# Performance work log

Hardware: AMD Instinct MI355X
Metric: run time of the kernel (lower is better)

Reference implementation:

```python
import jax, jax.numpy as jnp
import numpy as np

B, N, F, K = 4, 512, 128, 32
GAMMA = 10.0          # RBF width parameter
CUTOFF = 5.0          # RBF center range [0, CUTOFF]
LOG2 = 0.6931471805599453
EPS = 1e-12           # keeps sqrt grad finite on the (masked-out) diagonal


def ssp(x):
    # shifted softplus: ln(0.5*e^x + 0.5) = softplus(x) - ln 2
    return jax.nn.softplus(x) - LOG2


def setup_inputs() -> dict:
    key = jax.random.key(0)
    ks = jax.random.split(key, 8)
    coordinates = jax.random.normal(ks[0], (B, N, 3), dtype=jnp.float32) * 3.0
    atom_emb = jax.random.normal(ks[1], (B, N, F), dtype=jnp.float32)
    rbf_centers = jnp.linspace(0.0, CUTOFF, K, dtype=jnp.float32)
    # cfconv filter-generator dense layers
    w1 = jax.random.normal(ks[2], (K, F), dtype=jnp.float32) / np.float32(np.sqrt(K))
    b1 = jnp.zeros((F,), dtype=jnp.float32)
    w2 = jax.random.normal(ks[3], (F, F), dtype=jnp.float32) / np.float32(np.sqrt(F))
    b2 = jnp.zeros((F,), dtype=jnp.float32)
    # self.W linear (nn.Linear stores weight as [out, in])
    Ww = jax.random.normal(ks[4], (F, F), dtype=jnp.float32) / np.float32(np.sqrt(F))
    Wb = jnp.zeros((F,), dtype=jnp.float32)
    return {"coordinates": coordinates, "atom_emb": atom_emb,
            "rbf_centers": rbf_centers, "w1": w1, "b1": b1,
            "w2": w2, "b2": b2, "Ww": Ww, "Wb": Wb}


def reference(coordinates, atom_emb, rbf_centers, w1, b1, w2, b2, Ww, Wb):
    n = coordinates.shape[-2]
    # pairwise distances [B, N, N]
    diff = coordinates[:, :, None, :] - coordinates[:, None, :, :]
    d = jnp.sqrt(jnp.sum(diff * diff, axis=-1) + EPS)
    # Gaussian RBF expansion [B, N, N, K]
    rbf = jnp.exp(-GAMMA * (d[..., None] - rbf_centers) ** 2)
    # filter generator: Dense -> SSP -> Dense -> SSP  => W [B, N, N, F]
    Wf = ssp(jnp.einsum('bnmk,kf->bnmf', rbf, w1) + b1)
    Wf = ssp(jnp.einsum('bnmf,fg->bnmg', Wf, w2) + b2)
    # zero the diagonal (no self-interaction)
    mask = (1.0 - jnp.eye(n, dtype=Wf.dtype))[None, :, :, None]
    Wf = Wf * mask
    # x = self.W(atom_emb)
    x = atom_emb @ Ww.T + Wb
    # per-channel weighted neighbor aggregation
    x = jnp.einsum('bnmf,bmf->bnf', Wf, x)
    return atom_emb + x
```

## Files before the change

### kernel.cpp

```cpp
#include <hip/hip_runtime.h>
#include <hip/hip_bf16.h>

#define B_ 4
#define N_ 512
#define F_ 128
#define K_ 32
#define TD 2048
#define DMAX 6.5f
#define XWB (B_ * N_ / 2)
#define TKEEPI 1890

typedef __attribute__((ext_vector_type(4))) float f32x4;

__device__ __forceinline__ unsigned cvt_pk_bf16(float a, float b) {
  unsigned r;
  asm("v_cvt_pk_bf16_f32 %0, %1, %2" : "=v"(r) : "v"(a), "v"(b));
  return r;
}
__device__ __forceinline__ unsigned short f2bf1(float a) {
  return (unsigned short)cvt_pk_bf16(a, a);
}
__device__ __forceinline__ float exp2_hw(float x) {
  float r; asm("v_exp_f32 %0, %1" : "=v"(r) : "v"(x)); return r;
}
__device__ __forceinline__ float log2_hw(float x) {
  float r; asm("v_log_f32 %0, %1" : "=v"(r) : "v"(x)); return r;
}
__device__ __forceinline__ float lo16f(unsigned w) {
  return __builtin_bit_cast(float, w << 16);
}
__device__ __forceinline__ float hi16f(unsigned w) {
  return __builtin_bit_cast(float, w & 0xffff0000u);
}

__device__ __forceinline__ float sspb(float u) {
  float e = exp2_hw(__builtin_fabsf(u) * -1.4426950408889634f);
  float l = log2_hw(fmaf(e, 0.5f, 0.5f));
  return fmaf(l, 0.6931471805599453f, fmaxf(u, 0.f));
}

__launch_bounds__(256)
__global__ void prep_kernel(const float* __restrict__ emb, const float* __restrict__ Ww,
                            const float* __restrict__ Wb,
                            const float* __restrict__ w1, const float* __restrict__ b1,
                            const float* __restrict__ w2, const float* __restrict__ b2,
                            unsigned short* __restrict__ xbf,
                            unsigned short* __restrict__ tabn) {
  __shared__ float erow[2][F_];
  __shared__ float rbf_s[2][K_];
  __shared__ float h1s[2][F_];

  if (blockIdx.x < XWB) {
    const int r0 = blockIdx.x * 2;
    const int half = threadIdx.x >> 7, f = threadIdx.x & 127;
    erow[half][f] = emb[(r0 + half) * F_ + f];
    __syncthreads();
    const float4* w4 = (const float4*)(Ww + f * F_);
    const float* er = erow[half];
    float acc = 0.f;
#pragma unroll 8
    for (int g4 = 0; g4 < F_ / 4; ++g4) {
      float4 wv = w4[g4];
      acc = fmaf(er[g4 * 4 + 0], wv.x, acc);
      acc = fmaf(er[g4 * 4 + 1], wv.y, acc);
      acc = fmaf(er[g4 * 4 + 2], wv.z, acc);
      acc = fmaf(er[g4 * 4 + 3], wv.w, acc);
    }
    xbf[(r0 + half) * F_ + f] = f2bf1(acc + Wb[f]);
  } else {
    const int j = blockIdx.x - XWB;
    const int sl = threadIdx.x >> 7, f = threadIdx.x & 127;
    const int i = 2 * j + sl;
    const float d = (float)i * (DMAX / (float)(TD - 1));
    if (f < K_) {
      float t = d - (float)f * (5.0f / 31.0f);
      rbf_s[sl][f] = exp2_hw(t * t * -14.426950408889634f);
    }
    __syncthreads();
    float a1 = b1[f];
#pragma unroll 8
    for (int k = 0; k < K_; ++k) a1 = fmaf(rbf_s[sl][k], w1[k * F_ + f], a1);
    h1s[sl][f] = sspb(a1);
    __syncthreads();
    float a2 = b2[f];
#pragma unroll 8
    for (int g = 0; g < F_; ++g) a2 = fmaf(h1s[sl][g], w2[g * F_ + f], a2);
    tabn[i * F_ + f] = f2bf1(sspb(a2));
  }
}

__launch_bounds__(256, 5)
__global__ void agg_kernel(const float* __restrict__ coords, const float* __restrict__ emb,
                           const unsigned short* __restrict__ xbf,
                           const unsigned short* __restrict__ tabn,
                           float* __restrict__ out) {
  __shared__ unsigned cidx[N_ + 96];
  __shared__ unsigned wcnt[4];
  __shared__ float part[16][F_ + 4];

  const int blk = blockIdx.x;
  const int b = blk >> 9, n = blk & 511;
  const int tid = threadIdx.x;
  const int lane = tid & 63, wq = tid >> 6;

  const float cx = coords[(b * N_ + n) * 3 + 0];
  const float cy = coords[(b * N_ + n) * 3 + 1];
  const float cz = coords[(b * N_ + n) * 3 + 2];

  const float SC = (float)(TD - 1) / DMAX;
  const int mA = wq * 128 + lane;
  const int mB = mA + 64;
  unsigned vA, vB;
  bool keepA, keepB;
  {
    const float* cm = coords + (b * N_ + mA) * 3;
    float dx = cm[0] - cx, dy = cm[1] - cy, dz = cm[2] - cz;
    float d = sqrtf(fmaf(dx, dx, fmaf(dy, dy, fmaf(dz, dz, 1e-12f))));
    int ti = (int)fminf(fmaf(d, SC, 0.5f), (float)(TD - 1));
    vA = ((unsigned)ti << 16) | (unsigned)mA;
    keepA = (ti < TKEEPI) && (mA != n);
  }
  {
    const float* cm = coords + (b * N_ + mB) * 3;
    float dx = cm[0] - cx, dy = cm[1] - cy, dz = cm[2] - cz;
    float d = sqrtf(fmaf(dx, dx, fmaf(dy, dy, fmaf(dz, dz, 1e-12f))));
    int ti = (int)fminf(fmaf(d, SC, 0.5f), (float)(TD - 1));
    vB = ((unsigned)ti << 16) | (unsigned)mB;
    keepB = (ti < TKEEPI) && (mB != n);
  }
  unsigned long long bA = __ballot(keepA);
  unsigned long long bB = __ballot(keepB);
  if (lane == 0) wcnt[wq] = (unsigned)(__popcll(bA) + __popcll(bB));
  __syncthreads();
  const unsigned c0 = wcnt[0], c1 = wcnt[1], c2 = wcnt[2], c3 = wcnt[3];
  const int cnt = (int)(c0 + c1 + c2 + c3);
  {
    unsigned pre = (wq > 0 ? c0 : 0u) + (wq > 1 ? c1 : 0u) + (wq > 2 ? c2 : 0u);
    unsigned long long below = (1ull << lane) - 1ull;
    unsigned posA = pre + (unsigned)__popcll(bA & below);
    unsigned posB = pre + (unsigned)__popcll(bA) + (unsigned)__popcll(bB & below);
    if (keepA) cidx[posA] = vA;
    if (keepB) cidx[posB] = vB;
    if (tid < 96) cidx[cnt + tid] = ((unsigned)(TD - 1)) << 16;
  }
  __syncthreads();

  const int mg = tid >> 4;
  const int f0 = (tid & 15) * 8;
  const unsigned short* xp = xbf + b * N_ * F_ + f0;
  const unsigned short* tp = tabn + f0;

  f32x4 acc0 = {0.f, 0.f, 0.f, 0.f};
  f32x4 acc1 = {0.f, 0.f, 0.f, 0.f};

#define LOADP(V, T, X)                                                       \
  {                                                                          \
    unsigned v_ = (V);                                                       \
    T = *(const uint4*)(tp + (v_ >> 16) * F_);                               \
    X = *(const uint4*)(xp + (v_ & 0xffffu) * F_);                           \
  }
#define MAC8(T, X)                                                           \
  {                                                                          \
    acc0[0] = fmaf(lo16f(T.x), lo16f(X.x), acc0[0]);                         \
    acc0[1] = fmaf(hi16f(T.x), hi16f(X.x), acc0[1]);                         \
    acc0[2] = fmaf(lo16f(T.y), lo16f(X.y), acc0[2]);                         \
    acc0[3] = fmaf(hi16f(T.y), hi16f(X.y), acc0[3]);                         \
    acc1[0] = fmaf(lo16f(T.z), lo16f(X.z), acc1[0]);                         \
    acc1[1] = fmaf(hi16f(T.z), hi16f(X.z), acc1[1]);                         \
    acc1[2] = fmaf(lo16f(T.w), lo16f(X.w), acc1[2]);                         \
    acc1[3] = fmaf(hi16f(T.w), hi16f(X.w), acc1[3]);                         \
  }

  uint4 tA, xA, tB, xB, tC, xC, tD, xD;
  LOADP(cidx[mg], tA, xA)
  LOADP(cidx[mg + 16], tB, xB)
  LOADP(cidx[mg + 32], tC, xC)
  LOADP(cidx[mg + 48], tD, xD)
  int k = mg;
#pragma unroll 1
  while (k < cnt) {
    uint4 tE, xE, tF, xF;
    LOADP(cidx[k + 64], tE, xE)
    LOADP(cidx[k + 80], tF, xF)
    MAC8(tA, xA)
    MAC8(tB, xB)
    tA = tC; xA = xC; tB = tD; xB = xD;
    tC = tE; xC = xE; tD = tF; xD = xF;
    k += 32;
  }
#undef LOADP
#undef MAC8

  *(f32x4*)&part[mg][f0] = acc0;
  *(f32x4*)&part[mg][f0 + 4] = acc1;
  __syncthreads();

  if (tid < F_) {
    float s = 0.f;
#pragma unroll
    for (int g = 0; g < 16; ++g) s += part[g][tid];
    int o = (b * N_ + n) * F_ + tid;
    out[o] = emb[o] + s;
  }
}

extern "C" void kernel_launch(void* const* d_in, const int* in_sizes, int n_in,
                              void* d_out, int out_size, void* d_ws, size_t ws_size,
                              hipStream_t stream) {
  const float* coords = (const float*)d_in[0];
  const float* emb    = (const float*)d_in[1];
  const float* w1 = (const float*)d_in[3];
  const float* b1 = (const float*)d_in[4];
  const float* w2 = (const float*)d_in[5];
  const float* b2 = (const float*)d_in[6];
  const float* Ww = (const float*)d_in[7];
  const float* Wb = (const float*)d_in[8];
  float* out = (float*)d_out;

  unsigned short* xbf  = (unsigned short*)d_ws;
  unsigned short* tabn = xbf + B_ * N_ * F_;

  hipLaunchKernelGGL(prep_kernel, dim3(XWB + TD / 2), dim3(256), 0, stream,
                     emb, Ww, Wb, w1, b1, w2, b2, xbf, tabn);
  hipLaunchKernelGGL(agg_kernel, dim3(B_ * N_), dim3(256), 0, stream,
                     coords, emb, xbf, tabn, out);
}
```

Before: 39.09 us.

## Move neighbor-list compaction from aggregation kernel into prep kernel

The per-atom distance computation, cutoff test and ballot-based compaction of neighbor indices now run as extra blocks in the prep kernel, writing a compacted list per atom to workspace. The aggregation kernel only copies that list into shared memory before its gather-accumulate loop. The aim is to take the distance and compaction latency off the aggregation kernel's critical path, letting it overlap with the table and projection work. In exchange the list makes a round trip through global memory and the prep kernel gets more blocks.

```diff
diff --git a/kernel.cpp b/kernel.cpp
--- a/kernel.cpp
+++ b/kernel.cpp
@@ -8,7 +8,10 @@
 #define TD 2048
 #define DMAX 6.5f
 #define XWB (B_ * N_ / 2)
+#define TABB (TD / 2)
 #define TKEEPI 1890
+#define CL_STRIDE 640
+#define NSENT 96
 
 typedef __attribute__((ext_vector_type(4))) float f32x4;
 
@@ -40,15 +43,18 @@
 }
 
 __launch_bounds__(256)
-__global__ void prep_kernel(const float* __restrict__ emb, const float* __restrict__ Ww,
+__global__ void prep_kernel(const float* __restrict__ coords,
+                            const float* __restrict__ emb, const float* __restrict__ Ww,
                             const float* __restrict__ Wb,
                             const float* __restrict__ w1, const float* __restrict__ b1,
                             const float* __restrict__ w2, const float* __restrict__ b2,
                             unsigned short* __restrict__ xbf,
-                            unsigned short* __restrict__ tabn) {
+                            unsigned short* __restrict__ tabn,
+                            unsigned* __restrict__ clist) {
   __shared__ float erow[2][F_];
   __shared__ float rbf_s[2][K_];
   __shared__ float h1s[2][F_];
+  __shared__ unsigned wcnt[4];
 
   if (blockIdx.x < XWB) {
     const int r0 = blockIdx.x * 2;
@@ -67,7 +73,7 @@
       acc = fmaf(er[g4 * 4 + 3], wv.w, acc);
     }
     xbf[(r0 + half) * F_ + f] = f2bf1(acc + Wb[f]);
-  } else {
+  } else if (blockIdx.x < XWB + TABB) {
     const int j = blockIdx.x - XWB;
     const int sl = threadIdx.x >> 7, f = threadIdx.x & 127;
     const int i = 2 * j + sl;
@@ -86,63 +92,72 @@
 #pragma unroll 8
     for (int g = 0; g < F_; ++g) a2 = fmaf(h1s[sl][g], w2[g * F_ + f], a2);
     tabn[i * F_ + f] = f2bf1(sspb(a2));
-  }
-}
-
-__launch_bounds__(256, 5)
-__global__ void agg_kernel(const float* __restrict__ coords, const float* __restrict__ emb,
-                           const unsigned short* __restrict__ xbf,
-                           const unsigned short* __restrict__ tabn,
-                           float* __restrict__ out) {
-  __shared__ unsigned cidx[N_ + 96];
-  __shared__ unsigned wcnt[4];
-  __shared__ float part[16][F_ + 4];
-
-  const int blk = blockIdx.x;
-  const int b = blk >> 9, n = blk & 511;
-  const int tid = threadIdx.x;
-  const int lane = tid & 63, wq = tid >> 6;
-
-  const float cx = coords[(b * N_ + n) * 3 + 0];
-  const float cy = coords[(b * N_ + n) * 3 + 1];
-  const float cz = coords[(b * N_ + n) * 3 + 2];
-
-  const float SC = (float)(TD - 1) / DMAX;
-  const int mA = wq * 128 + lane;
-  const int mB = mA + 64;
-  unsigned vA, vB;
-  bool keepA, keepB;
-  {
-    const float* cm = coords + (b * N_ + mA) * 3;
-    float dx = cm[0] - cx, dy = cm[1] - cy, dz = cm[2] - cz;
-    float d = sqrtf(fmaf(dx, dx, fmaf(dy, dy, fmaf(dz, dz, 1e-12f))));
-    int ti = (int)fminf(fmaf(d, SC, 0.5f), (float)(TD - 1));
-    vA = ((unsigned)ti << 16) | (unsigned)mA;
-    keepA = (ti < TKEEPI) && (mA != n);
-  }
-  {
-    const float* cm = coords + (b * N_ + mB) * 3;
-    float dx = cm[0] - cx, dy = cm[1] - cy, dz = cm[2] - cz;
-    float d = sqrtf(fmaf(dx, dx, fmaf(dy, dy, fmaf(dz, dz, 1e-12f))));
-    int ti = (int)fminf(fmaf(d, SC, 0.5f), (float)(TD - 1));
-    vB = ((unsigned)ti << 16) | (unsigned)mB;
-    keepB = (ti < TKEEPI) && (mB != n);
-  }
-  unsigned long long bA = __ballot(keepA);
-  unsigned long long bB = __ballot(keepB);
-  if (lane == 0) wcnt[wq] = (unsigned)(__popcll(bA) + __popcll(bB));
-  __syncthreads();
-  const unsigned c0 = wcnt[0], c1 = wcnt[1], c2 = wcnt[2], c3 = wcnt[3];
-  const int cnt = (int)(c0 + c1 + c2 + c3);
-  {
+  } else {
+    const int j2 = blockIdx.x - (XWB + TABB);
+    const int b = j2 >> 9, n = j2 & 511;
+    const int tid = threadIdx.x;
+    const int lane = tid & 63, wq = tid >> 6;
+    unsigned* cl = clist + j2 * CL_STRIDE;
+
+    const float cx = coords[(b * N_ + n) * 3 + 0];
+    const float cy = coords[(b * N_ + n) * 3 + 1];
+    const float cz = coords[(b * N_ + n) * 3 + 2];
+
+    const float SC = (float)(TD - 1) / DMAX;
+    const int mA = wq * 128 + lane;
+    const int mB = mA + 64;
+    unsigned vA, vB;
+    bool keepA, keepB;
+    {
+      const float* cm = coords + (b * N_ + mA) * 3;
+      float dx = cm[0] - cx, dy = cm[1] - cy, dz = cm[2] - cz;
+      float d = sqrtf(fmaf(dx, dx, fmaf(dy, dy, fmaf(dz, dz, 1e-12f))));
+      int ti = (int)fminf(fmaf(d, SC, 0.5f), (float)(TD - 1));
+      vA = ((unsigned)ti << 16) | (unsigned)mA;
+      keepA = (ti < TKEEPI) && (mA != n);
+    }
+    {
+      const float* cm = coords + (b * N_ + mB) * 3;
+      float dx = cm[0] - cx, dy = cm[1] - cy, dz = cm[2] - cz;
+      float d = sqrtf(fmaf(dx, dx, fmaf(dy, dy, fmaf(dz, dz, 1e-12f))));
+      int ti = (int)fminf(fmaf(d, SC, 0.5f), (float)(TD - 1));
+      vB = ((unsigned)ti << 16) | (unsigned)mB;
+      keepB = (ti < TKEEPI) && (mB != n);
+    }
+    unsigned long long bA = __ballot(keepA);
+    unsigned long long bB = __ballot(keepB);
+    if (lane == 0) wcnt[wq] = (unsigned)(__popcll(bA) + __popcll(bB));
+    __syncthreads();
+    const unsigned c0 = wcnt[0], c1 = wcnt[1], c2 = wcnt[2], c3 = wcnt[3];
+    const unsigned cnt = c0 + c1 + c2 + c3;
     unsigned pre = (wq > 0 ? c0 : 0u) + (wq > 1 ? c1 : 0u) + (wq > 2 ? c2 : 0u);
     unsigned long long below = (1ull << lane) - 1ull;
     unsigned posA = pre + (unsigned)__popcll(bA & below);
     unsigned posB = pre + (unsigned)__popcll(bA) + (unsigned)__popcll(bB & below);
-    if (keepA) cidx[posA] = vA;
-    if (keepB) cidx[posB] = vB;
-    if (tid < 96) cidx[cnt + tid] = ((unsigned)(TD - 1)) << 16;
-  }
+    if (keepA) cl[1 + posA] = vA;
+    if (keepB) cl[1 + posB] = vB;
+    if (tid < NSENT) cl[1 + cnt + tid] = ((unsigned)(TD - 1)) << 16;
+    if (tid == 0) cl[0] = cnt;
+  }
+}
+
+__launch_bounds__(256, 5)
+__global__ void agg_kernel(const float* __restrict__ emb,
+                           const unsigned short* __restrict__ xbf,
+                           const unsigned short* __restrict__ tabn,
+                           const unsigned* __restrict__ clist,
+                           float* __restrict__ out) {
+  __shared__ unsigned cidx[N_ + NSENT];
+  __shared__ float part[16][F_ + 4];
+
+  const int blk = blockIdx.x;
+  const int b = blk >> 9;
+  const int tid = threadIdx.x;
+
+  const unsigned* cl = clist + blk * CL_STRIDE;
+  const int cnt = (int)cl[0];
+  for (int i = tid; i < cnt + NSENT; i += 256)
+    cidx[i] = cl[1 + i];
   __syncthreads();
 
   const int mg = tid >> 4;
@@ -199,7 +214,7 @@
     float s = 0.f;
 #pragma unroll
     for (int g = 0; g < 16; ++g) s += part[g][tid];
-    int o = (b * N_ + n) * F_ + tid;
+    int o = blk * F_ + tid;
     out[o] = emb[o] + s;
   }
 }
@@ -219,9 +234,10 @@
 
   unsigned short* xbf  = (unsigned short*)d_ws;
   unsigned short* tabn = xbf + B_ * N_ * F_;
-
-  hipLaunchKernelGGL(prep_kernel, dim3(XWB + TD / 2), dim3(256), 0, stream,
-                     emb, Ww, Wb, w1, b1, w2, b2, xbf, tabn);
+  unsigned* clist = (unsigned*)(tabn + TD * F_);
+
+  hipLaunchKernelGGL(prep_kernel, dim3(XWB + TABB + B_ * N_), dim3(256), 0, stream,
+                     coords, emb, Ww, Wb, w1, b1, w2, b2, xbf, tabn, clist);
   hipLaunchKernelGGL(agg_kernel, dim3(B_ * N_), dim3(256), 0, stream,
-                     coords, emb, xbf, tabn, out);
-}
+                     emb, xbf, tabn, clist, out);
+}
```

Measured after the change: 39.26 us. No clear change (+0.4%).
